# Performance work log

Measured on AMD Instinct MI355X. Metric: run time of the kernel, lower is better.

Reference implementation:

```python
import jax, jax.numpy as jnp
import numpy as np

RWKV_K_CLAMP = 60.0
B, T, C = 8, 1024, 1024
LAYER_ID, N_LAYER = 2, 12


def _decay_speed():
    # replicate RWKV_TimeMix.__init__ decay_speed construction
    first = 1
    f1 = 3.0 + (LAYER_ID - first) / (N_LAYER - 1 - first) * (1.2 - 3.0)
    f2 = 0.65 + (LAYER_ID - first) / (N_LAYER - 1 - first) * (0.4 - 0.65)
    if LAYER_ID == first:
        f1 += 0.5
    if LAYER_ID == N_LAYER - 2:
        f2 = 0.4
    if LAYER_ID == N_LAYER - 1:
        f2 = 0.37
    h = np.arange(C, dtype=np.float64)
    return (f2 ** (h / (C - 1) * 7.0)) * f1


def setup_inputs() -> dict:
    key = jax.random.key(0)
    ks = jax.random.split(key, 6)
    scale = 1.0 / np.sqrt(C)
    time_mix = np.ones((C,), np.float32)
    time_mix[: C // 2] = 0.0
    return {
        "x": jax.random.normal(ks[0], (B, T, C), jnp.float32),
        "time_decay": jnp.asarray(np.log(_decay_speed()), jnp.float32),  # (C,)
        "time_first": jnp.full((C,), np.log(0.3), jnp.float32),
        "time_mix": jnp.asarray(time_mix),
        "combined_mix": jnp.full((C,), 0.01, jnp.float32),
        "Wk": jax.random.normal(ks[1], (C, C), jnp.float32) * scale,
        "Wv": jax.random.normal(ks[2], (C, C), jnp.float32) * scale,
        "Wr": jax.random.normal(ks[3], (C, C), jnp.float32) * scale,
        "Wo": jax.random.normal(ks[4], (C, C), jnp.float32) * scale,
    }


def _wkv(w, u, k, v):
    # w,u: (C,); k,v: (B,T,C). Numerically-stable decayed linear recurrence
    # (RWKV wkv kernel: running-max, like online softmax).
    b = k.shape[0]
    init = (
        jnp.zeros((b, C), k.dtype),            # numerator state a
        jnp.zeros((b, C), k.dtype),            # denominator state b
        jnp.full((b, C), -1e38, k.dtype),      # running max exponent p
    )

    def step(carry, kv):
        a, bb, p = carry
        kt, vt = kv  # (B,C)
        no = jnp.maximum(p, u + kt)
        e1 = jnp.exp(p - no)
        e2 = jnp.exp(u + kt - no)
        y = (e1 * a + e2 * vt) / (e1 * bb + e2)
        no2 = jnp.maximum(w + p, kt)
        e1 = jnp.exp(w + p - no2)
        e2 = jnp.exp(kt - no2)
        return (e1 * a + e2 * vt, e1 * bb + e2, no2), y

    _, y = jax.lax.scan(step, init, (k.transpose(1, 0, 2), v.transpose(1, 0, 2)))
    return y.transpose(1, 0, 2)  # (B,T,C)


def reference(x, time_decay, time_first, time_mix, combined_mix, Wk, Wv, Wr, Wo):
    b, t, c = x.shape
    zrow = jnp.zeros((b, 1, c), x.dtype)
    x_m1 = jnp.concatenate([zrow, x[:, :-1, :]], axis=1)   # time_shift / x_{t-1}
    x_p1 = jnp.concatenate([x[:, 1:, :], zrow], axis=1)    # x_{t+1}
    half = c // 2
    x_comb = jnp.concatenate([x_m1[:, :, :half], x_p1[:, :, half:]], axis=-1)
    xm = x * time_mix + x_m1 * (1.0 - time_mix) + x_comb * combined_mix
    k = jnp.exp(jnp.minimum(jnp.einsum("btc,dc->btd", xm, Wk), RWKV_K_CLAMP))
    v = jnp.einsum("btc,dc->btd", xm, Wv)
    r = jnp.einsum("btc,dc->btd", xm, Wr)
    wkv = _wkv(time_decay / t, time_first / t, k, v)
    return jnp.einsum("btc,dc->btd", jax.nn.sigmoid(r) * wkv, Wo)
```

## Files before the change

kernel.cpp:

```cpp
#include <hip/hip_runtime.h>
#include <hip/hip_bf16.h>
#include <stdint.h>

#define B_SZ 8
#define T_LEN 1024
#define C_DIM 1024
#define M_ROWS (B_SZ * T_LEN)
#define NCH 32
#define CHL (T_LEN / NCH)

typedef unsigned short ushort_t;
typedef __attribute__((ext_vector_type(8))) short short8;
typedef __attribute__((ext_vector_type(4))) float f32x4;
typedef __attribute__((ext_vector_type(4))) unsigned short us4;

static __device__ __forceinline__ float bf2f(ushort_t u) {
  union { unsigned int i; float f; } x; x.i = ((unsigned int)u) << 16; return x.f;
}
static __device__ __forceinline__ ushort_t f2bf(float f) {
  union { float f; unsigned int i; } x; x.f = f;
  unsigned int r = x.i + 0x7fffu + ((x.i >> 16) & 1u);
  return (ushort_t)(r >> 16);
}

static __device__ __forceinline__ void gload_lds16(const void* g, void* l) {
  __builtin_amdgcn_global_load_lds(
      (const __attribute__((address_space(1))) void*)g,
      (__attribute__((address_space(3))) void*)l, 16, 0, 0);
}

__global__ void cvt_w_kernel(const float* __restrict__ wk, const float* __restrict__ wv,
                             const float* __restrict__ wr, const float* __restrict__ wo,
                             ushort_t* __restrict__ out) {
  int gid = blockIdx.x * 256 + threadIdx.x;
  int which = gid >> 18;
  int off = (gid << 2) & ((1 << 20) - 1);
  const float* src = which == 0 ? wk : which == 1 ? wv : which == 2 ? wr : wo;
  float4 v = *(const float4*)(src + off);
  us4 o = {f2bf(v.x), f2bf(v.y), f2bf(v.z), f2bf(v.w)};
  *(us4*)(out + (size_t)gid * 4) = o;
}

__global__ void xm_kernel(const float* __restrict__ x, const float* __restrict__ tm,
                          const float* __restrict__ cm, ushort_t* __restrict__ xmb) {
  int gid = blockIdx.x * 256 + threadIdx.x;
  int c4 = (gid & (C_DIM / 4 - 1)) * 4;
  int t = (gid >> 8) & (T_LEN - 1);
  const float4 zero = {0.f, 0.f, 0.f, 0.f};
  float4 xv = *(const float4*)(x + (size_t)gid * 4);
  float4 xp = (t > 0) ? *(const float4*)(x + (size_t)gid * 4 - C_DIM) : zero;
  float4 xn = (t < T_LEN - 1) ? *(const float4*)(x + (size_t)gid * 4 + C_DIM) : zero;
  float4 tmv = *(const float4*)(tm + c4);
  float4 cmv = *(const float4*)(cm + c4);
  float4 xc = (c4 < C_DIM / 2) ? xp : xn;
  us4 o;
  o.x = f2bf(xv.x * tmv.x + xp.x * (1.f - tmv.x) + xc.x * cmv.x);
  o.y = f2bf(xv.y * tmv.y + xp.y * (1.f - tmv.y) + xc.y * cmv.y);
  o.z = f2bf(xv.z * tmv.z + xp.z * (1.f - tmv.z) + xc.z * cmv.z);
  o.w = f2bf(xv.w * tmv.w + xp.w * (1.f - tmv.w) + xc.w * cmv.w);
  *(us4*)(xmb + (size_t)gid * 4) = o;
}

template <int FUSED, int BN>
__global__ __launch_bounds__(256) void gemm_bt(const ushort_t* __restrict__ A,
                                               const ushort_t* __restrict__ Bw,
                                               float* __restrict__ outF,
                                               ushort_t* __restrict__ outV,
                                               ushort_t* __restrict__ outR) {
  constexpr int K = 1024;
  constexpr int NT = K / 32;
  constexpr int NF = BN / 32;
  __shared__ ushort_t As[2][128 * 32];
  __shared__ ushort_t Bs[2][BN * 32];

  const int tid = threadIdx.x;
  const int lane = tid & 63;
  const int wave = tid >> 6;
  const int bm = blockIdx.x * 128;
  const int jb = blockIdx.y;
  const int mode = FUSED ? (jb >> 3) : 3;
  const int bn = FUSED ? (jb & 7) * BN : jb * BN;
  const ushort_t* Bp = FUSED ? (Bw + ((size_t)(jb >> 3) << 20)) : Bw;

  const int wr = (wave >> 1) * 64;
  const int wc = (wave & 1) * (BN / 2);

  f32x4 acc[4][NF];
#pragma unroll
  for (int m = 0; m < 4; ++m)
#pragma unroll
    for (int n = 0; n < NF; ++n) acc[m][n] = (f32x4){0.f, 0.f, 0.f, 0.f};

  const int srow = tid >> 2;
  const int scol = (((tid & 3) ^ ((srow >> 1) & 3)) * 8);
  const ushort_t* Ag = A + (size_t)(bm + srow) * K + scol;
  const ushort_t* Bg = Bp + (size_t)(bn + srow) * K + scol;
  ushort_t* AsP0 = &As[0][tid * 8];
  ushort_t* BsP0 = &Bs[0][tid * 8];
  ushort_t* AsP1 = &As[1][tid * 8];
  ushort_t* BsP1 = &Bs[1][tid * 8];

  const int fr = lane & 15;
  const int kq = lane >> 4;
  const int ps = (kq ^ ((fr >> 1) & 3)) * 8;

  auto stage = [&](int buf, int k0) {
    ushort_t* ap = buf ? AsP1 : AsP0;
    ushort_t* bp = buf ? BsP1 : BsP0;
    gload_lds16(Ag + k0, ap);
    gload_lds16(Ag + (size_t)64 * K + k0, ap + 64 * 32);
    gload_lds16(Bg + k0, bp);
    if (BN == 128) gload_lds16(Bg + (size_t)64 * K + k0, bp + 64 * 32);
  };

  stage(0, 0);
  asm volatile("s_waitcnt vmcnt(0)" ::: "memory");
  __syncthreads();

  int cur = 0;
  for (int t = 0; t < NT; ++t) {
    if (t < NT - 1) stage(cur ^ 1, (t + 1) * 32);
    short8 af[4], bfr[NF];
#pragma unroll
    for (int m = 0; m < 4; ++m)
      af[m] = *(const short8*)&As[cur][(wr + m * 16 + fr) * 32 + ps];
#pragma unroll
    for (int n = 0; n < NF; ++n)
      bfr[n] = *(const short8*)&Bs[cur][(wc + n * 16 + fr) * 32 + ps];
#pragma unroll
    for (int m = 0; m < 4; ++m)
#pragma unroll
      for (int n = 0; n < NF; ++n)
        acc[m][n] = __builtin_amdgcn_mfma_f32_16x16x32_bf16(af[m], bfr[n], acc[m][n], 0, 0, 0);
    asm volatile("s_waitcnt vmcnt(0)" ::: "memory");
    __syncthreads();
    cur ^= 1;
  }

  const int crow0 = (lane >> 4) * 4;
#pragma unroll
  for (int m = 0; m < 4; ++m)
#pragma unroll
    for (int n = 0; n < NF; ++n)
#pragma unroll
      for (int j = 0; j < 4; ++j) {
        float v = acc[m][n][j];
        size_t idx = (size_t)(bm + wr + m * 16 + crow0 + j) * C_DIM + (bn + wc + n * 16 + fr);
        if (mode == 0) {
          outF[idx] = __expf(fminf(v, 60.f));
        } else if (mode == 1) {
          outV[idx] = f2bf(v);
        } else if (mode == 2) {
          outR[idx] = f2bf(1.f / (1.f + __expf(-v)));
        } else {
          outF[idx] = v;
        }
      }
}

__global__ void wkv_phaseA(const float* __restrict__ kk, const ushort_t* __restrict__ vv,
                           const float* __restrict__ td,
                           float* __restrict__ sa, float* __restrict__ sb,
                           float* __restrict__ sp) {
  int gid = blockIdx.x * 256 + threadIdx.x;
  int c = gid & (C_DIM - 1);
  int ch = (gid >> 10) & (NCH - 1);
  int b = gid >> 15;
  float w = td[c] * (1.f / T_LEN);
  size_t base = ((size_t)b * T_LEN + ch * CHL) * C_DIM + c;
  float a = 0.f, bb = 0.f, p = -1e38f;
  for (int t = 0; t < CHL; ++t) {
    float kt = kk[base + (size_t)t * C_DIM];
    float vt = bf2f(vv[base + (size_t)t * C_DIM]);
    float no2 = fmaxf(w + p, kt);
    float e1 = __expf(w + p - no2);
    float e2 = __expf(kt - no2);
    a = e1 * a + e2 * vt;
    bb = e1 * bb + e2;
    p = no2;
  }
  sa[gid] = a; sb[gid] = bb; sp[gid] = p;
}

__global__ void wkv_phaseB(const float* __restrict__ td,
                           float* __restrict__ sa, float* __restrict__ sb,
                           float* __restrict__ sp) {
  int gid = blockIdx.x * 256 + threadIdx.x;
  int c = gid & (C_DIM - 1);
  int b = gid >> 10;
  float wL = td[c] * (1.f / T_LEN) * (float)CHL;
  float a = 0.f, bb = 0.f, p = -1e38f;
  for (int ch = 0; ch < NCH; ++ch) {
    size_t idx = ((size_t)b * NCH + ch) * C_DIM + c;
    float ac = sa[idx], bc = sb[idx], pc = sp[idx];
    sa[idx] = a; sb[idx] = bb; sp[idx] = p;
    float pn = fmaxf(p + wL, pc);
    float e1 = __expf(p + wL - pn);
    float e2 = __expf(pc - pn);
    a = e1 * a + e2 * ac;
    bb = e1 * bb + e2 * bc;
    p = pn;
  }
}

__global__ void wkv_phaseC(const float* __restrict__ kk, const ushort_t* __restrict__ vv,
                           const ushort_t* __restrict__ sr, const float* __restrict__ td,
                           const float* __restrict__ tf,
                           const float* __restrict__ sa, const float* __restrict__ sb,
                           const float* __restrict__ sp, ushort_t* __restrict__ sy) {
  int gid = blockIdx.x * 256 + threadIdx.x;
  int c = gid & (C_DIM - 1);
  int ch = (gid >> 10) & (NCH - 1);
  int b = gid >> 15;
  float w = td[c] * (1.f / T_LEN);
  float u = tf[c] * (1.f / T_LEN);
  size_t base = ((size_t)b * T_LEN + ch * CHL) * C_DIM + c;
  float a = sa[gid], bb = sb[gid], p = sp[gid];
  for (int t = 0; t < CHL; ++t) {
    float kt = kk[base + (size_t)t * C_DIM];
    float vt = bf2f(vv[base + (size_t)t * C_DIM]);
    float no = fmaxf(p, u + kt);
    float e1 = __expf(p - no);
    float e2 = __expf(u + kt - no);
    float y = (e1 * a + e2 * vt) / (e1 * bb + e2);
    float srv = bf2f(sr[base + (size_t)t * C_DIM]);
    sy[base + (size_t)t * C_DIM] = f2bf(srv * y);
    float no2 = fmaxf(w + p, kt);
    e1 = __expf(w + p - no2);
    e2 = __expf(kt - no2);
    a = e1 * a + e2 * vt;
    bb = e1 * bb + e2;
    p = no2;
  }
}

extern "C" void kernel_launch(void* const* d_in, const int* in_sizes, int n_in,
                              void* d_out, int out_size, void* d_ws, size_t ws_size,
                              hipStream_t stream) {
  const float* x  = (const float*)d_in[0];
  const float* td = (const float*)d_in[1];
  const float* tf = (const float*)d_in[2];
  const float* tm = (const float*)d_in[3];
  const float* cm = (const float*)d_in[4];
  const float* Wk = (const float*)d_in[5];
  const float* Wv = (const float*)d_in[6];
  const float* Wr = (const float*)d_in[7];
  const float* Wo = (const float*)d_in[8];

  const size_t MC = (size_t)M_ROWS * C_DIM;
  const size_t CC = (size_t)C_DIM * C_DIM;

  char* ws = (char*)d_ws;
  ushort_t* xmb = (ushort_t*)ws; ws += MC * 2;
  ushort_t* Wb  = (ushort_t*)ws; ws += 4 * CC * 2;
  float*    kk  = (float*)ws;    ws += MC * 4;
  ushort_t* vv  = (ushort_t*)ws; ws += MC * 2;
  ushort_t* sr  = (ushort_t*)ws; ws += MC * 2;
  ushort_t* sy  = (ushort_t*)ws; ws += MC * 2;
  float* sa = (float*)ws; ws += (size_t)B_SZ * NCH * C_DIM * 4;
  float* sb = (float*)ws; ws += (size_t)B_SZ * NCH * C_DIM * 4;
  float* sp = (float*)ws; ws += (size_t)B_SZ * NCH * C_DIM * 4;

  cvt_w_kernel<<<(4 * CC / 4) / 256, 256, 0, stream>>>(Wk, Wv, Wr, Wo, Wb);
  xm_kernel<<<(MC / 4) / 256, 256, 0, stream>>>(x, tm, cm, xmb);

  gemm_bt<1, 128><<<dim3(M_ROWS / 128, 24), 256, 0, stream>>>(xmb, Wb, kk, vv, sr);

  wkv_phaseA<<<(B_SZ * NCH * C_DIM) / 256, 256, 0, stream>>>(kk, vv, td, sa, sb, sp);
  wkv_phaseB<<<(B_SZ * C_DIM) / 256, 256, 0, stream>>>(td, sa, sb, sp);
  wkv_phaseC<<<(B_SZ * NCH * C_DIM) / 256, 256, 0, stream>>>(kk, vv, sr, td, tf, sa, sb, sp, sy);

  gemm_bt<0, 64><<<dim3(M_ROWS / 128, 16), 256, 0, stream>>>(sy, Wb + 3 * CC, (float*)d_out, nullptr, nullptr);
}
```

Baseline: 168.4 us.

## Replace fused KVR GEMM with 256x256-tile pipelined 8-wave MFMA kernel

The fused K/V/R projection GEMM moves from 128x128 tiles with 4 waves and a single-stage double buffer to 256x256 tiles with 8 waves and 64-wide K steps. Global-to-LDS loads are split into quarter stages interleaved with MFMA sub-blocks, synchronised by explicit barriers, vmcnt waits and setprio. A grid swizzle is added for L2 locality. The goal is higher arithmetic intensity and better overlap of loads with MFMA work, at the cost of many more registers and a large LDS footprint, which limits occupancy to 2 blocks per CU.

Result: no change. 171.2 us (+1.6%).

```diff
diff --git a/kernel.cpp b/kernel.cpp
--- a/kernel.cpp
+++ b/kernel.cpp
@@ -61,14 +61,175 @@
   *(us4*)(xmb + (size_t)gid * 4) = o;
 }
 
-template <int FUSED, int BN>
-__global__ __launch_bounds__(256) void gemm_bt(const ushort_t* __restrict__ A,
-                                               const ushort_t* __restrict__ Bw,
-                                               float* __restrict__ outF,
-                                               ushort_t* __restrict__ outV,
-                                               ushort_t* __restrict__ outR) {
+
+#define RDA(buf, mh)                                                          \
+  {                                                                           \
+    _Pragma("unroll") for (int mq = 0; mq < 4; ++mq) {                        \
+      _Pragma("unroll") for (int ks = 0; ks < 2; ++ks) {                      \
+        const int row = ((mh)*4 + mq) * 32 + wm * 16 + fr;                    \
+        const int cp = ((ks * 4 + kq) ^ (fr & 7)) * 8;                        \
+        a_fr[mq][ks] = *(const short8*)&lds[buf][0][row * 64 + cp];           \
+      }                                                                       \
+    }                                                                         \
+  }
+
+#define RDB(buf, nh)                                                          \
+  {                                                                           \
+    _Pragma("unroll") for (int nq = 0; nq < 2; ++nq) {                        \
+      _Pragma("unroll") for (int ks = 0; ks < 2; ++ks) {                      \
+        const int row = ((nh)*2 + nq) * 64 + wn * 16 + fr;                    \
+        const int cp = ((ks * 4 + kq) ^ (fr & 7)) * 8;                        \
+        b_fr[(nh)*2 + nq][ks] = *(const short8*)&lds[buf][1][row * 64 + cp];  \
+      }                                                                       \
+    }                                                                         \
+  }
+
+#define DOMFMA(mh, nh)                                                        \
+  {                                                                           \
+    _Pragma("unroll") for (int mq = 0; mq < 4; ++mq) {                        \
+      _Pragma("unroll") for (int nq = 0; nq < 2; ++nq) {                      \
+        _Pragma("unroll") for (int ks = 0; ks < 2; ++ks) {                    \
+          acc[(mh)*4 + mq][(nh)*2 + nq] =                                     \
+              __builtin_amdgcn_mfma_f32_16x16x32_bf16(                        \
+                  a_fr[mq][ks], b_fr[(nh)*2 + nq][ks],                        \
+                  acc[(mh)*4 + mq][(nh)*2 + nq], 0, 0, 0);                    \
+        }                                                                     \
+      }                                                                       \
+    }                                                                         \
+  }
+
+#define VM6 asm volatile("s_waitcnt vmcnt(6)" ::: "memory");
+#define VM0 asm volatile("s_waitcnt vmcnt(0)" ::: "memory");
+
+#define MFMA_BLOCK(mh, nh, VMW)                                               \
+  __builtin_amdgcn_s_barrier();                                               \
+  asm volatile("s_waitcnt lgkmcnt(0)" ::: "memory");                          \
+  __builtin_amdgcn_sched_barrier(0);                                          \
+  __builtin_amdgcn_s_setprio(1);                                              \
+  DOMFMA(mh, nh);                                                             \
+  __builtin_amdgcn_s_setprio(0);                                              \
+  VMW                                                                         \
+  __builtin_amdgcn_s_barrier();                                               \
+  __builtin_amdgcn_sched_barrier(0);
+
+__global__ __launch_bounds__(512, 2) void gemm256(const ushort_t* __restrict__ A,
+                                                  const ushort_t* __restrict__ Bw,
+                                                  float* __restrict__ outK,
+                                                  ushort_t* __restrict__ outV,
+                                                  ushort_t* __restrict__ outR) {
+  __shared__ ushort_t lds[2][2][16384];
+
+  const int tid = threadIdx.x;
+  const int lane = tid & 63;
+  const int wid = tid >> 6;
+  const int wm = wid >> 2;
+  const int wn = wid & 3;
+  const int fr = lane & 15;
+  const int kq = lane >> 4;
+
+  const int lid = blockIdx.x;
+  const int swz = (lid & 7) * 48 + (lid >> 3);
+  const int bm = (swz & 31) * 256;
+  const int jb = swz >> 5;
+  const int mode = jb >> 2;
+  const int bn = (jb & 3) * 256;
+  const ushort_t* Bp = Bw + ((size_t)mode << 20);
+
+  f32x4 acc[8][4];
+#pragma unroll
+  for (int m = 0; m < 8; ++m)
+#pragma unroll
+    for (int n = 0; n < 4; ++n) acc[m][n] = (f32x4){0.f, 0.f, 0.f, 0.f};
+
+  short8 a_fr[4][2];
+  short8 b_fr[4][2];
+
+  const int srow = tid >> 3;
+  const int scol = ((tid & 7) ^ (srow & 7)) * 8;
+  const ushort_t* Ag = A + (size_t)(bm + srow) * 1024 + scol;
+  const ushort_t* Bg = Bp + (size_t)(bn + srow) * 1024 + scol;
+
+  auto stage = [&](int buf, int kt, int s) {
+    const int op = (s == 1 || s == 3) ? 1 : 0;
+    const int h = (s == 1 || s == 2) ? 1 : 0;
+    const ushort_t* g = (op ? Bg : Ag) + (size_t)(h * 128) * 1024 + kt * 64;
+    ushort_t* dst = &lds[buf][op][h * 8192 + tid * 8];
+    gload_lds16(g, dst);
+    gload_lds16(g + 64 * 1024, dst + 4096);
+  };
+
+  stage(0, 0, 0); stage(0, 0, 1); stage(0, 0, 2); stage(0, 0, 3);
+  stage(1, 1, 0); stage(1, 1, 1); stage(1, 1, 2);
+  VM6
+  __builtin_amdgcn_s_barrier();
+
+#pragma unroll 1
+  for (int i = 0; i < 7; ++i) {
+    const int kt = 2 * i;
+    RDA(0, 0) RDB(0, 0)
+    stage(1, kt + 1, 3);
+    MFMA_BLOCK(0, 0, )
+    RDB(0, 1)
+    stage(0, kt + 2, 0);
+    MFMA_BLOCK(0, 1, )
+    RDA(0, 1)
+    stage(0, kt + 2, 1);
+    MFMA_BLOCK(1, 1, )
+    stage(0, kt + 2, 2);
+    MFMA_BLOCK(1, 0, VM6)
+    RDA(1, 0) RDB(1, 0)
+    stage(0, kt + 2, 3);
+    MFMA_BLOCK(0, 0, )
+    RDB(1, 1)
+    stage(1, kt + 3, 0);
+    MFMA_BLOCK(0, 1, )
+    RDA(1, 1)
+    stage(1, kt + 3, 1);
+    MFMA_BLOCK(1, 1, )
+    stage(1, kt + 3, 2);
+    MFMA_BLOCK(1, 0, VM6)
+  }
+  RDA(0, 0) RDB(0, 0)
+  stage(1, 15, 3);
+  MFMA_BLOCK(0, 0, )
+  RDB(0, 1)
+  MFMA_BLOCK(0, 1, )
+  RDA(0, 1)
+  MFMA_BLOCK(1, 1, )
+  MFMA_BLOCK(1, 0, VM0)
+  RDA(1, 0) RDB(1, 0)
+  MFMA_BLOCK(0, 0, )
+  RDB(1, 1)
+  MFMA_BLOCK(0, 1, )
+  RDA(1, 1)
+  MFMA_BLOCK(1, 1, )
+  DOMFMA(1, 0)
+
+#pragma unroll
+  for (int mf = 0; mf < 8; ++mf)
+#pragma unroll
+    for (int nf = 0; nf < 4; ++nf)
+#pragma unroll
+      for (int j = 0; j < 4; ++j) {
+        float v = acc[mf][nf][j];
+        size_t idx = (size_t)(bm + mf * 32 + wm * 16 + kq * 4 + j) * C_DIM +
+                     (bn + nf * 64 + wn * 16 + fr);
+        if (mode == 0) {
+          outK[idx] = __expf(fminf(v, 60.f));
+        } else if (mode == 1) {
+          outV[idx] = f2bf(v);
+        } else {
+          outR[idx] = f2bf(1.f / (1.f + __expf(-v)));
+        }
+      }
+}
+
+__global__ __launch_bounds__(256) void gemm_out(const ushort_t* __restrict__ A,
+                                                const ushort_t* __restrict__ Bw,
+                                                float* __restrict__ outF) {
   constexpr int K = 1024;
   constexpr int NT = K / 32;
+  constexpr int BN = 64;
   constexpr int NF = BN / 32;
   __shared__ ushort_t As[2][128 * 32];
   __shared__ ushort_t Bs[2][BN * 32];
@@ -77,10 +238,7 @@
   const int lane = tid & 63;
   const int wave = tid >> 6;
   const int bm = blockIdx.x * 128;
-  const int jb = blockIdx.y;
-  const int mode = FUSED ? (jb >> 3) : 3;
-  const int bn = FUSED ? (jb & 7) * BN : jb * BN;
-  const ushort_t* Bp = FUSED ? (Bw + ((size_t)(jb >> 3) << 20)) : Bw;
+  const int bn = blockIdx.y * BN;
 
   const int wr = (wave >> 1) * 64;
   const int wc = (wave & 1) * (BN / 2);
@@ -94,7 +252,7 @@
   const int srow = tid >> 2;
   const int scol = (((tid & 3) ^ ((srow >> 1) & 3)) * 8);
   const ushort_t* Ag = A + (size_t)(bm + srow) * K + scol;
-  const ushort_t* Bg = Bp + (size_t)(bn + srow) * K + scol;
+  const ushort_t* Bg = Bw + (size_t)(bn + srow) * K + scol;
   ushort_t* AsP0 = &As[0][tid * 8];
   ushort_t* BsP0 = &Bs[0][tid * 8];
   ushort_t* AsP1 = &As[1][tid * 8];
@@ -110,7 +268,6 @@
     gload_lds16(Ag + k0, ap);
     gload_lds16(Ag + (size_t)64 * K + k0, ap + 64 * 32);
     gload_lds16(Bg + k0, bp);
-    if (BN == 128) gload_lds16(Bg + (size_t)64 * K + k0, bp + 64 * 32);
   };
 
   stage(0, 0);
@@ -143,19 +300,9 @@
 #pragma unroll
     for (int n = 0; n < NF; ++n)
 #pragma unroll
-      for (int j = 0; j < 4; ++j) {
-        float v = acc[m][n][j];
-        size_t idx = (size_t)(bm + wr + m * 16 + crow0 + j) * C_DIM + (bn + wc + n * 16 + fr);
-        if (mode == 0) {
-          outF[idx] = __expf(fminf(v, 60.f));
-        } else if (mode == 1) {
-          outV[idx] = f2bf(v);
-        } else if (mode == 2) {
-          outR[idx] = f2bf(1.f / (1.f + __expf(-v)));
-        } else {
-          outF[idx] = v;
-        }
-      }
+      for (int j = 0; j < 4; ++j)
+        outF[(size_t)(bm + wr + m * 16 + crow0 + j) * C_DIM + (bn + wc + n * 16 + fr)] =
+            acc[m][n][j];
 }
 
 __global__ void wkv_phaseA(const float* __restrict__ kk, const ushort_t* __restrict__ vv,
@@ -264,11 +411,11 @@
   cvt_w_kernel<<<(4 * CC / 4) / 256, 256, 0, stream>>>(Wk, Wv, Wr, Wo, Wb);
   xm_kernel<<<(MC / 4) / 256, 256, 0, stream>>>(x, tm, cm, xmb);
 
-  gemm_bt<1, 128><<<dim3(M_ROWS / 128, 24), 256, 0, stream>>>(xmb, Wb, kk, vv, sr);
+  gemm256<<<dim3(384), 512, 0, stream>>>(xmb, Wb, kk, vv, sr);
 
   wkv_phaseA<<<(B_SZ * NCH * C_DIM) / 256, 256, 0, stream>>>(kk, vv, td, sa, sb, sp);
   wkv_phaseB<<<(B_SZ * C_DIM) / 256, 256, 0, stream>>>(td, sa, sb, sp);
   wkv_phaseC<<<(B_SZ * NCH * C_DIM) / 256, 256, 0, stream>>>(kk, vv, sr, td, tf, sa, sb, sp, sy);
 
-  gemm_bt<0, 64><<<dim3(M_ROWS / 128, 16), 256, 0, stream>>>(sy, Wb + 3 * CC, (float*)d_out, nullptr, nullptr);
-}
+  gemm_out<<<dim3(M_ROWS / 128, C_DIM / 64), 256, 0, stream>>>(sy, Wb + 3 * CC, (float*)d_out);
+}
```

## Fuse WKV chunk-prefix scan into phase C and remap GEMM blocks per XCD

Applied to the files above, without the earlier changes.

Removes the separate sequential phase-B kernel. Each phase-C thread now recomputes its own prefix over earlier chunk states (up to 31 steps), which trades redundant work for one fewer launch and one fewer pass through the state arrays. The GEMMs switch to a 1D grid with an XCD-aware block swizzle so that neighbouring M tiles land on the same XCD for better L2 reuse. The output GEMM also moves from BN=64 to BN=128 tiles, which halves its block count to 512.

Result: no change. 166.0 us (-1.4%).

```diff
diff --git a/kernel.cpp b/kernel.cpp
--- a/kernel.cpp
+++ b/kernel.cpp
@@ -61,7 +61,7 @@
   *(us4*)(xmb + (size_t)gid * 4) = o;
 }
 
-template <int FUSED, int BN>
+template <int FUSED>
 __global__ __launch_bounds__(256) void gemm_bt(const ushort_t* __restrict__ A,
                                                const ushort_t* __restrict__ Bw,
                                                float* __restrict__ outF,
@@ -69,27 +69,30 @@
                                                ushort_t* __restrict__ outR) {
   constexpr int K = 1024;
   constexpr int NT = K / 32;
-  constexpr int NF = BN / 32;
   __shared__ ushort_t As[2][128 * 32];
-  __shared__ ushort_t Bs[2][BN * 32];
+  __shared__ ushort_t Bs[2][128 * 32];
 
   const int tid = threadIdx.x;
   const int lane = tid & 63;
   const int wave = tid >> 6;
-  const int bm = blockIdx.x * 128;
-  const int jb = blockIdx.y;
+
+  const int bid = blockIdx.x;
+  const int xcd = bid & 7;
+  const int r = bid >> 3;
+  const int bm = (xcd * 8 + (r & 7)) * 128;
+  const int jb = r >> 3;
   const int mode = FUSED ? (jb >> 3) : 3;
-  const int bn = FUSED ? (jb & 7) * BN : jb * BN;
+  const int bn = FUSED ? (jb & 7) * 128 : jb * 128;
   const ushort_t* Bp = FUSED ? (Bw + ((size_t)(jb >> 3) << 20)) : Bw;
 
   const int wr = (wave >> 1) * 64;
-  const int wc = (wave & 1) * (BN / 2);
-
-  f32x4 acc[4][NF];
+  const int wc = (wave & 1) * 64;
+
+  f32x4 acc[4][4];
 #pragma unroll
   for (int m = 0; m < 4; ++m)
 #pragma unroll
-    for (int n = 0; n < NF; ++n) acc[m][n] = (f32x4){0.f, 0.f, 0.f, 0.f};
+    for (int n = 0; n < 4; ++n) acc[m][n] = (f32x4){0.f, 0.f, 0.f, 0.f};
 
   const int srow = tid >> 2;
   const int scol = (((tid & 3) ^ ((srow >> 1) & 3)) * 8);
@@ -110,7 +113,7 @@
     gload_lds16(Ag + k0, ap);
     gload_lds16(Ag + (size_t)64 * K + k0, ap + 64 * 32);
     gload_lds16(Bg + k0, bp);
-    if (BN == 128) gload_lds16(Bg + (size_t)64 * K + k0, bp + 64 * 32);
+    gload_lds16(Bg + (size_t)64 * K + k0, bp + 64 * 32);
   };
 
   stage(0, 0);
@@ -120,17 +123,17 @@
   int cur = 0;
   for (int t = 0; t < NT; ++t) {
     if (t < NT - 1) stage(cur ^ 1, (t + 1) * 32);
-    short8 af[4], bfr[NF];
+    short8 af[4], bfr[4];
 #pragma unroll
     for (int m = 0; m < 4; ++m)
       af[m] = *(const short8*)&As[cur][(wr + m * 16 + fr) * 32 + ps];
 #pragma unroll
-    for (int n = 0; n < NF; ++n)
+    for (int n = 0; n < 4; ++n)
       bfr[n] = *(const short8*)&Bs[cur][(wc + n * 16 + fr) * 32 + ps];
 #pragma unroll
     for (int m = 0; m < 4; ++m)
 #pragma unroll
-      for (int n = 0; n < NF; ++n)
+      for (int n = 0; n < 4; ++n)
         acc[m][n] = __builtin_amdgcn_mfma_f32_16x16x32_bf16(af[m], bfr[n], acc[m][n], 0, 0, 0);
     asm volatile("s_waitcnt vmcnt(0)" ::: "memory");
     __syncthreads();
@@ -141,7 +144,7 @@
 #pragma unroll
   for (int m = 0; m < 4; ++m)
 #pragma unroll
-    for (int n = 0; n < NF; ++n)
+    for (int n = 0; n < 4; ++n)
 #pragma unroll
       for (int j = 0; j < 4; ++j) {
         float v = acc[m][n][j];
@@ -182,18 +185,25 @@
   sa[gid] = a; sb[gid] = bb; sp[gid] = p;
 }
 
-__global__ void wkv_phaseB(const float* __restrict__ td,
-                           float* __restrict__ sa, float* __restrict__ sb,
-                           float* __restrict__ sp) {
+__global__ void wkv_phaseC2(const float* __restrict__ kk, const ushort_t* __restrict__ vv,
+                            const ushort_t* __restrict__ sr, const float* __restrict__ td,
+                            const float* __restrict__ tf,
+                            const float* __restrict__ sa, const float* __restrict__ sb,
+                            const float* __restrict__ sp, ushort_t* __restrict__ sy) {
   int gid = blockIdx.x * 256 + threadIdx.x;
   int c = gid & (C_DIM - 1);
-  int b = gid >> 10;
-  float wL = td[c] * (1.f / T_LEN) * (float)CHL;
+  int ch = (gid >> 10) & (NCH - 1);
+  int b = gid >> 15;
+  float w = td[c] * (1.f / T_LEN);
+  float u = tf[c] * (1.f / T_LEN);
+  float wL = w * (float)CHL;
+
   float a = 0.f, bb = 0.f, p = -1e38f;
-  for (int ch = 0; ch < NCH; ++ch) {
-    size_t idx = ((size_t)b * NCH + ch) * C_DIM + c;
-    float ac = sa[idx], bc = sb[idx], pc = sp[idx];
-    sa[idx] = a; sb[idx] = bb; sp[idx] = p;
+  size_t sbase = ((size_t)b * NCH) * C_DIM + c;
+  for (int j = 0; j < ch; ++j) {
+    float ac = sa[sbase + (size_t)j * C_DIM];
+    float bc = sb[sbase + (size_t)j * C_DIM];
+    float pc = sp[sbase + (size_t)j * C_DIM];
     float pn = fmaxf(p + wL, pc);
     float e1 = __expf(p + wL - pn);
     float e2 = __expf(pc - pn);
@@ -201,21 +211,8 @@
     bb = e1 * bb + e2 * bc;
     p = pn;
   }
-}
-
-__global__ void wkv_phaseC(const float* __restrict__ kk, const ushort_t* __restrict__ vv,
-                           const ushort_t* __restrict__ sr, const float* __restrict__ td,
-                           const float* __restrict__ tf,
-                           const float* __restrict__ sa, const float* __restrict__ sb,
-                           const float* __restrict__ sp, ushort_t* __restrict__ sy) {
-  int gid = blockIdx.x * 256 + threadIdx.x;
-  int c = gid & (C_DIM - 1);
-  int ch = (gid >> 10) & (NCH - 1);
-  int b = gid >> 15;
-  float w = td[c] * (1.f / T_LEN);
-  float u = tf[c] * (1.f / T_LEN);
+
   size_t base = ((size_t)b * T_LEN + ch * CHL) * C_DIM + c;
-  float a = sa[gid], bb = sb[gid], p = sp[gid];
   for (int t = 0; t < CHL; ++t) {
     float kt = kk[base + (size_t)t * C_DIM];
     float vt = bf2f(vv[base + (size_t)t * C_DIM]);
@@ -264,11 +261,10 @@
   cvt_w_kernel<<<(4 * CC / 4) / 256, 256, 0, stream>>>(Wk, Wv, Wr, Wo, Wb);
   xm_kernel<<<(MC / 4) / 256, 256, 0, stream>>>(x, tm, cm, xmb);
 
-  gemm_bt<1, 128><<<dim3(M_ROWS / 128, 24), 256, 0, stream>>>(xmb, Wb, kk, vv, sr);
+  gemm_bt<1><<<dim3(1536), 256, 0, stream>>>(xmb, Wb, kk, vv, sr);
 
   wkv_phaseA<<<(B_SZ * NCH * C_DIM) / 256, 256, 0, stream>>>(kk, vv, td, sa, sb, sp);
-  wkv_phaseB<<<(B_SZ * C_DIM) / 256, 256, 0, stream>>>(td, sa, sb, sp);
-  wkv_phaseC<<<(B_SZ * NCH * C_DIM) / 256, 256, 0, stream>>>(kk, vv, sr, td, tf, sa, sb, sp, sy);
-
-  gemm_bt<0, 64><<<dim3(M_ROWS / 128, 16), 256, 0, stream>>>(sy, Wb + 3 * CC, (float*)d_out, nullptr, nullptr);
-}
+  wkv_phaseC2<<<(B_SZ * NCH * C_DIM) / 256, 256, 0, stream>>>(kk, vv, sr, td, tf, sa, sb, sp, sy);
+
+  gemm_bt<0><<<dim3(512), 256, 0, stream>>>(sy, Wb + 3 * CC, (float*)d_out, nullptr, nullptr);
+}
```
